# Performance work log

Measured on AMD Instinct MI355X. Metric: run time of the kernel, lower is better.

The kernel has to match this reference:

```python
import jax, jax.numpy as jnp
import numpy as np

B, T, I, H, L = 32768, 30, 4, 64, 32


def _lstm_layer(x, Wih, Whh, bih, bhh):
    """PyTorch-semantics single-layer LSTM, batch_first. Returns (outputs [B,T,H], h_T [B,H])."""
    # Precompute input contribution for all timesteps: [B, T, 4H]
    xg = jnp.einsum('bti,gi->btg', x, Wih) + bih + bhh
    Hh = Whh.shape[1]
    h0 = jnp.zeros((x.shape[0], Hh), x.dtype)

    def step(carry, xg_t):
        h, c = carry
        g = xg_t + h @ Whh.T  # [B, 4H]
        i, f, gg, o = jnp.split(g, 4, axis=-1)  # PyTorch gate order i,f,g,o
        c = jax.nn.sigmoid(f) * c + jax.nn.sigmoid(i) * jnp.tanh(gg)
        h = jax.nn.sigmoid(o) * jnp.tanh(c)
        return (h, c), h

    (hT, _), hs = jax.lax.scan(step, (h0, h0), jnp.swapaxes(xg, 0, 1))
    return jnp.swapaxes(hs, 0, 1), hT


def setup_inputs() -> dict:
    key = jax.random.key(0)
    ks = jax.random.split(key, 20)
    s = 0.1  # weight scale for numerical stability
    inp = {
        'x': jax.random.normal(ks[0], (B, T, I), jnp.float32),
        'enc1_Wih': s * jax.random.normal(ks[1], (4 * H, I), jnp.float32),
        'enc1_Whh': s * jax.random.normal(ks[2], (4 * H, H), jnp.float32),
        'enc1_bih': s * jax.random.normal(ks[3], (4 * H,), jnp.float32),
        'enc1_bhh': s * jax.random.normal(ks[4], (4 * H,), jnp.float32),
        'enc2_Wih': s * jax.random.normal(ks[5], (4 * L, H), jnp.float32),
        'enc2_Whh': s * jax.random.normal(ks[6], (4 * L, L), jnp.float32),
        'enc2_bih': s * jax.random.normal(ks[7], (4 * L,), jnp.float32),
        'enc2_bhh': s * jax.random.normal(ks[8], (4 * L,), jnp.float32),
        'dec1_Wih': s * jax.random.normal(ks[9], (4 * H, L), jnp.float32),
        'dec1_Whh': s * jax.random.normal(ks[10], (4 * H, H), jnp.float32),
        'dec1_bih': s * jax.random.normal(ks[11], (4 * H,), jnp.float32),
        'dec1_bhh': s * jax.random.normal(ks[12], (4 * H,), jnp.float32),
        'dec2_Wih': s * jax.random.normal(ks[13], (4 * I, H), jnp.float32),
        'dec2_Whh': s * jax.random.normal(ks[14], (4 * I, I), jnp.float32),
        'dec2_bih': s * jax.random.normal(ks[15], (4 * I,), jnp.float32),
        'dec2_bhh': s * jax.random.normal(ks[16], (4 * I,), jnp.float32),
    }
    return inp


def reference(x, enc1_Wih, enc1_Whh, enc1_bih, enc1_bhh,
              enc2_Wih, enc2_Whh, enc2_bih, enc2_bhh,
              dec1_Wih, dec1_Whh, dec1_bih, dec1_bhh,
              dec2_Wih, dec2_Whh, dec2_bih, dec2_bhh):
    seq_len = x.shape[1]
    out, _ = _lstm_layer(x, enc1_Wih, enc1_Whh, enc1_bih, enc1_bhh)
    out, h = _lstm_layer(out, enc2_Wih, enc2_Whh, enc2_bih, enc2_bhh)
    latent = jnp.repeat(h[:, None, :], seq_len, axis=1)  # [B, T, L]
    out, _ = _lstm_layer(latent, dec1_Wih, dec1_Whh, dec1_bih, dec1_bhh)
    out, _ = _lstm_layer(out, dec2_Wih, dec2_Whh, dec2_bih, dec2_bhh)
    return out
```

## Files before the change

### kernel.cpp

```cpp
#include <hip/hip_runtime.h>
#include <stdint.h>


typedef unsigned short u16;
typedef unsigned int u32;
typedef __attribute__((ext_vector_type(8))) short bf16x8;
typedef __attribute__((ext_vector_type(4))) short s16x4;
typedef __attribute__((ext_vector_type(4))) float f32x4;

#define BATCH 32768
#define TT 30
#define IN 4
#define WAVES 16
#define BLOCKT (WAVES * 64)
#define MB 16
#define NPAIR 8
#define BPB (NPAIR * MB)

#define LOG2E 1.4426950408889634f
#define LOG2E2 2.8853900817779268f

#define WREG 18432
#define O_WHH1HI 0
#define O_W1FOLD 8192
#define O_WIH2HI 12288
#define O_WHH2HI 16384
#define O_WHH3HI 0
#define O_WIH3HI 8192
#define O_WIH4HI 12288
#define O_W4HHF  12800

#define NBIAS 400
#define PBUF 1600
#define SMEM_WORDS (WREG + NBIAS + NPAIR * PBUF)
#define SMEM_BYTES (SMEM_WORDS * 4)

#define WB() __builtin_amdgcn_wave_barrier()
#define MFMA(a, b, c) __builtin_amdgcn_mfma_f32_16x16x32_bf16((a), (b), (c), 0, 0, 0)

__device__ __forceinline__ u16 f2bf(float f) {
    u32 u = __float_as_uint(f);
    u += 0x7fffu + ((u >> 16) & 1u);
    return (u16)(u >> 16);
}
__device__ __forceinline__ float bf2f(u16 v) { return __uint_as_float(((u32)v) << 16); }
__device__ __forceinline__ float sigY(float y) {
    return __builtin_amdgcn_rcpf(1.f + __builtin_amdgcn_exp2f(-y));
}
__device__ __forceinline__ float tanhY(float y) {
    return fmaf(-2.f, __builtin_amdgcn_rcpf(__builtin_amdgcn_exp2f(y) + 1.f), 1.f);
}
__device__ __forceinline__ float tanhC(float c) { return tanhY(c * LOG2E2); }

template <int KT, int GS>
__device__ __forceinline__ void stageBh(u16* hi, const float* src, int N, int tid) {
    const int K = KT * 32;
    const int total = N * K;
    for (int idx = tid; idx < total; idx += BLOCKT) {
        const int j = idx & 7;
        const int l = (idx >> 3) & 63;
        const int pr = idx >> 9;
        const int kt = pr & (KT - 1);
        const int nt = pr / KT;
        const int n = (nt << 4) | (l & 15);
        const int k = (kt << 5) + ((l >> 4) << 3) + j;
        const float s = (((n >> GS) & 3) == 2) ? LOG2E2 : LOG2E;
        hi[idx] = f2bf(src[n * K + k] * s);
    }
}

__device__ __forceinline__ f32x4 splat4(float b) {
    f32x4 v = {b, b, b, b};
    return v;
}

__global__ __launch_bounds__(BLOCKT)
__attribute__((amdgpu_waves_per_eu(4, 4)))
void lstm_ae(
    const float* __restrict__ x,
    const float* __restrict__ w1ih, const float* __restrict__ w1hh,
    const float* __restrict__ b1i, const float* __restrict__ b1h,
    const float* __restrict__ w2ih, const float* __restrict__ w2hh,
    const float* __restrict__ b2i, const float* __restrict__ b2h,
    const float* __restrict__ w3ih, const float* __restrict__ w3hh,
    const float* __restrict__ b3i, const float* __restrict__ b3h,
    const float* __restrict__ w4ih, const float* __restrict__ w4hh,
    const float* __restrict__ b4i, const float* __restrict__ b4h,
    float* __restrict__ out) {
    extern __shared__ float smem[];
    float* W = smem;
    float* biasF = smem + WREG;
    float* bufs = biasF + NBIAS;

    const int tid = threadIdx.x;
    const int wave = tid >> 6, lane = tid & 63;
    const int pair = wave & 7, role = wave >> 3;
    const int col = lane & 15, quad = lane >> 4;

    float* pb = bufs + pair * PBUF;
    u16* h1d = (u16*)pb;
    u16* h2b = (u16*)(pb + 1024);
    u16* xfold = (u16*)(pb + 1280);
    float* gbuf = pb + 1280;
    float* bufH4 = pb + 1536;

    const int b0w = blockIdx.x * BPB + pair * MB;

    stageBh<2, 6>((u16*)(W + O_WHH1HI), w1hh, 256, tid);
    stageBh<2, 5>((u16*)(W + O_WIH2HI), w2ih, 128, tid);
    stageBh<1, 5>((u16*)(W + O_WHH2HI), w2hh, 128, tid);
    {
        u16* F = (u16*)(W + O_W1FOLD);
        for (int idx = tid; idx < 16 * 512; idx += BLOCKT) {
            const int nt = idx >> 9;
            const int rem = idx & 511;
            const int l = rem >> 3;
            const int j = rem & 7;
            const int q = l >> 4;
            const int n = (nt << 4) | (l & 15);
            const float s = ((n >> 6) == 2) ? LOG2E2 : LOG2E;
            u16 v = 0;
            if (q == 0) {
                v = f2bf(w1ih[n * 4 + (j & 3)] * s);
            } else if (q == 1) {
                if (j < 4) {
                    const float w = w1ih[n * 4 + j] * s;
                    v = f2bf(w - bf2f(f2bf(w)));
                } else if (j == 4) {
                    v = f2bf((b1i[n] + b1h[n]) * s);
                } else if (j == 5) {
                    const float b = (b1i[n] + b1h[n]) * s;
                    v = f2bf(b - bf2f(f2bf(b)));
                }
            }
            F[idx] = v;
        }
    }
    for (int i = tid; i < 128; i += BLOCKT)
        biasF[i] = (b2i[i] + b2h[i]) * ((((i >> 5) & 3) == 2) ? LOG2E2 : LOG2E);
    for (int i = tid; i < 256; i += BLOCKT)
        biasF[128 + i] = (b3i[i] + b3h[i]) * ((((i >> 6) & 3) == 2) ? LOG2E2 : LOG2E);
    for (int i = tid; i < 16; i += BLOCKT)
        biasF[384 + i] = (b4i[i] + b4h[i]) * ((((i >> 2) & 3) == 2) ? LOG2E2 : LOG2E);
    {
        u32* z = (u32*)pb;
        if (role == 0) {
            for (int i = lane; i < 1024; i += 64) z[i] = 0u;
            for (int i = lane; i < 256; i += 64) z[1280 + i] = 0u;
        } else {
            for (int i = lane; i < 256; i += 64) z[1024 + i] = 0u;
            if (lane < 64) bufH4[lane] = 0.f;
        }
    }
    WB();
    if (role == 0 && quad == 1) {
        xfold[lane * 8 + 4] = (u16)0x3F80;
        xfold[lane * 8 + 5] = (u16)0x3F80;
    }
    __syncthreads();

    const u16* Whh1hi = (const u16*)(W + O_WHH1HI);
    const u16* W1fold = (const u16*)(W + O_W1FOLD);
    const u16* Wih2hi = (const u16*)(W + O_WIH2HI);
    const u16* Whh2hi = (const u16*)(W + O_WHH2HI);

    float c1[4][4];
    float c2[2][4];
#pragma unroll
    for (int q = 0; q < 4; ++q)
#pragma unroll
        for (int r = 0; r < 4; ++r) c1[q][r] = 0.f;
#pragma unroll
    for (int q = 0; q < 2; ++q)
#pragma unroll
        for (int r = 0; r < 4; ++r) c2[q][r] = 0.f;

    const f32x4 zf = {0.f, 0.f, 0.f, 0.f};
    float4 xcur;
    if (role == 0)
        xcur = *reinterpret_cast<const float4*>(x + ((size_t)(b0w + col) * TT + 0) * IN);

    for (int s = 0; s <= TT; ++s) {
        if (role == 0) {
            if (s < TT) {
                {
                    const u16 xh0 = f2bf(xcur.x), xh1 = f2bf(xcur.y);
                    const u16 xh2 = f2bf(xcur.z), xh3 = f2bf(xcur.w);
                    if (quad == 0) {
                        bf16x8 v;
                        v[0] = (short)xh0; v[1] = (short)xh1; v[2] = (short)xh2; v[3] = (short)xh3;
                        v[4] = (short)f2bf(xcur.x - bf2f(xh0));
                        v[5] = (short)f2bf(xcur.y - bf2f(xh1));
                        v[6] = (short)f2bf(xcur.z - bf2f(xh2));
                        v[7] = (short)f2bf(xcur.w - bf2f(xh3));
                        *reinterpret_cast<bf16x8*>(xfold + lane * 8) = v;
                    } else if (quad == 1) {
                        s16x4 v;
                        v[0] = (short)xh0; v[1] = (short)xh1; v[2] = (short)xh2; v[3] = (short)xh3;
                        *reinterpret_cast<s16x4*>(xfold + lane * 8) = v;
                    }
                }
                WB();
                {
                    const int tn = (s + 1 < TT) ? s + 1 : s;
                    xcur = *reinterpret_cast<const float4*>(
                        x + ((size_t)(b0w + col) * TT + tn) * IN);
                }
                const u16* hprev = h1d + (((s + 1) & 1) << 10);
                u16* hout = h1d + ((s & 1) << 10);
                const bf16x8 a1h0 = *reinterpret_cast<const bf16x8*>(hprev + lane * 8);
                const bf16x8 a1h1 = *reinterpret_cast<const bf16x8*>(hprev + (64 + lane) * 8);
                const bf16x8 a1x = *reinterpret_cast<const bf16x8*>(xfold + lane * 8);
#pragma unroll
                for (int q = 0; q < 4; ++q) {
                    f32x4 acc[4];
#pragma unroll
                    for (int i = 0; i < 4; ++i) {
                        const int nt = i * 4 + q;
                        const bf16x8 bx = *reinterpret_cast<const bf16x8*>(W1fold + (nt * 64 + lane) * 8);
                        const bf16x8 bh0 = *reinterpret_cast<const bf16x8*>(Whh1hi + ((nt * 2 + 0) * 64 + lane) * 8);
                        const bf16x8 bh1 = *reinterpret_cast<const bf16x8*>(Whh1hi + ((nt * 2 + 1) * 64 + lane) * 8);
                        f32x4 a = MFMA(a1x, bx, zf);
                        a = MFMA(a1h0, bh0, a);
                        a = MFMA(a1h1, bh1, a);
                        acc[i] = a;
                    }
                    const int kt = q >> 1;
                    const int lup = ((((q & 1) << 1) + (col >> 3)) << 4);
                    const int j = col & 7;
#pragma unroll
                    for (int r = 0; r < 4; ++r) {
                        const int m = quad * 4 + r;
                        const float iv = sigY(acc[0][r]);
                        const float fv = sigY(acc[1][r]);
                        const float gv = tanhY(acc[2][r]);
                        const float ov = sigY(acc[3][r]);
                        c1[q][r] = fv * c1[q][r] + iv * gv;
                        const float h = ov * tanhC(c1[q][r]);
                        hout[(kt * 64 + m + lup) * 8 + j] = f2bf(h);
                    }
                }
            }
        } else {
            if (s >= 1) {
                const u16* hprev = h1d + (((s + 1) & 1) << 10);
                const bf16x8 a1h0 = *reinterpret_cast<const bf16x8*>(hprev + lane * 8);
                const bf16x8 a1h1 = *reinterpret_cast<const bf16x8*>(hprev + (64 + lane) * 8);
                const bf16x8 a2h = *reinterpret_cast<const bf16x8*>(h2b + lane * 8);
                f32x4 acc2[8];
#pragma unroll
                for (int nt = 0; nt < 8; ++nt) {
                    const bf16x8 bh0 = *reinterpret_cast<const bf16x8*>(Wih2hi + ((nt * 2 + 0) * 64 + lane) * 8);
                    const bf16x8 bh1 = *reinterpret_cast<const bf16x8*>(Wih2hi + ((nt * 2 + 1) * 64 + lane) * 8);
                    const bf16x8 ch = *reinterpret_cast<const bf16x8*>(Whh2hi + (nt * 64 + lane) * 8);
                    f32x4 a = splat4(biasF[nt * 16 + col]);
                    a = MFMA(a1h0, bh0, a);
                    a = MFMA(a1h1, bh1, a);
                    a = MFMA(a2h, ch, a);
                    acc2[nt] = a;
                }
                WB();
#pragma unroll
                for (int q = 0; q < 2; ++q) {
                    const int lup = (((q << 1) + (col >> 3)) << 4);
                    const int j = col & 7;
#pragma unroll
                    for (int r = 0; r < 4; ++r) {
                        const int m = quad * 4 + r;
                        const float iv = sigY(acc2[q][r]);
                        const float fv = sigY(acc2[2 + q][r]);
                        const float gv = tanhY(acc2[4 + q][r]);
                        const float ov = sigY(acc2[6 + q][r]);
                        c2[q][r] = fv * c2[q][r] + iv * gv;
                        const float h = ov * tanhC(c2[q][r]);
                        h2b[(m + lup) * 8 + j] = f2bf(h);
                    }
                }
            }
        }
        __syncthreads();
    }

    stageBh<2, 6>((u16*)(W + O_WHH3HI), w3hh, 256, tid);
    stageBh<1, 6>((u16*)(W + O_WIH3HI), w3ih, 256, tid);
    stageBh<2, 2>((u16*)(W + O_WIH4HI), w4ih, 16, tid);
    for (int i = tid; i < 64; i += BLOCKT)
        W[O_W4HHF + i] = w4hh[i] * ((((i >> 4) & 3) == 2) ? LOG2E2 : LOG2E);
    if (role == 0) {
        u32* z = (u32*)pb;
        for (int i = lane; i < 1024; i += 64) z[i] = 0u;
    } else {
        if (lane < 64) bufH4[lane] = 0.f;
    }
    __syncthreads();

    const u16* Whh3hi = (const u16*)(W + O_WHH3HI);
    const u16* Wih3hi = (const u16*)(W + O_WIH3HI);
    const u16* Wih4hi = (const u16*)(W + O_WIH4HI);
    const float* W4hhF = W + O_W4HHF;

    float c3[4][4];
    float c4 = 0.f, bias4r = 0.f;
    bf16x8 aLh;
    if (role == 0) {
#pragma unroll
        for (int q = 0; q < 4; ++q)
#pragma unroll
            for (int r = 0; r < 4; ++r) c3[q][r] = 0.f;
        aLh = *reinterpret_cast<const bf16x8*>(h2b + lane * 8);
    } else {
        bias4r = biasF[384 + col];
    }
    const int u4 = lane & 3, mb = lane >> 2;

    for (int s = 0; s <= TT; ++s) {
        if (role == 0) {
            if (s < TT) {
                const u16* hprev = h1d + (((s + 1) & 1) << 10);
                u16* hout = h1d + ((s & 1) << 10);
                const bf16x8 a3h0 = *reinterpret_cast<const bf16x8*>(hprev + lane * 8);
                const bf16x8 a3h1 = *reinterpret_cast<const bf16x8*>(hprev + (64 + lane) * 8);
#pragma unroll
                for (int q = 0; q < 4; ++q) {
                    f32x4 acc[4];
#pragma unroll
                    for (int i = 0; i < 4; ++i) {
                        const int nt = i * 4 + q;
                        const bf16x8 bL = *reinterpret_cast<const bf16x8*>(Wih3hi + (nt * 64 + lane) * 8);
                        const bf16x8 bh0 = *reinterpret_cast<const bf16x8*>(Whh3hi + ((nt * 2 + 0) * 64 + lane) * 8);
                        const bf16x8 bh1 = *reinterpret_cast<const bf16x8*>(Whh3hi + ((nt * 2 + 1) * 64 + lane) * 8);
                        f32x4 a = MFMA(aLh, bL, splat4(biasF[128 + nt * 16 + col]));
                        a = MFMA(a3h0, bh0, a);
                        a = MFMA(a3h1, bh1, a);
                        acc[i] = a;
                    }
                    const int kt = q >> 1;
                    const int lup = ((((q & 1) << 1) + (col >> 3)) << 4);
                    const int j = col & 7;
#pragma unroll
                    for (int r = 0; r < 4; ++r) {
                        const int m = quad * 4 + r;
                        const float iv = sigY(acc[0][r]);
                        const float fv = sigY(acc[1][r]);
                        const float gv = tanhY(acc[2][r]);
                        const float ov = sigY(acc[3][r]);
                        c3[q][r] = fv * c3[q][r] + iv * gv;
                        const float h = ov * tanhC(c3[q][r]);
                        hout[(kt * 64 + m + lup) * 8 + j] = f2bf(h);
                    }
                }
            }
        } else {
            if (s >= 1) {
                const int t = s - 1;
                const u16* hprev = h1d + (((s + 1) & 1) << 10);
                const bf16x8 a3h0 = *reinterpret_cast<const bf16x8*>(hprev + lane * 8);
                const bf16x8 a3h1 = *reinterpret_cast<const bf16x8*>(hprev + (64 + lane) * 8);
                f32x4 acc4 = splat4(bias4r);
                {
                    const float4 w4 = *reinterpret_cast<const float4*>(W4hhF + col * 4);
#pragma unroll
                    for (int r = 0; r < 4; ++r) {
                        const float4 hv = *reinterpret_cast<const float4*>(bufH4 + (quad * 4 + r) * 4);
                        float sa = acc4[r];
                        sa = fmaf(w4.x, hv.x, sa);
                        sa = fmaf(w4.y, hv.y, sa);
                        sa = fmaf(w4.z, hv.z, sa);
                        sa = fmaf(w4.w, hv.w, sa);
                        acc4[r] = sa;
                    }
                }
                {
                    const bf16x8 bh0 = *reinterpret_cast<const bf16x8*>(Wih4hi + (0 * 64 + lane) * 8);
                    const bf16x8 bh1 = *reinterpret_cast<const bf16x8*>(Wih4hi + (1 * 64 + lane) * 8);
                    acc4 = MFMA(a3h0, bh0, acc4);
                    acc4 = MFMA(a3h1, bh1, acc4);
                }
                WB();
#pragma unroll
                for (int r = 0; r < 4; ++r) gbuf[(quad * 4 + r) * 16 + col] = acc4[r];
                WB();
                {
                    const float iv = sigY(gbuf[mb * 16 + u4]);
                    const float fv = sigY(gbuf[mb * 16 + 4 + u4]);
                    const float gv = tanhY(gbuf[mb * 16 + 8 + u4]);
                    const float ov = sigY(gbuf[mb * 16 + 12 + u4]);
                    c4 = fv * c4 + iv * gv;
                    const float h = ov * tanhC(c4);
                    out[((size_t)(b0w + mb) * TT + t) * IN + u4] = h;
                    bufH4[mb * 4 + u4] = h;
                }
                WB();
            }
        }
        __syncthreads();
    }
}

extern "C" void kernel_launch(void* const* d_in, const int* in_sizes, int n_in,
                              void* d_out, int out_size, void* d_ws, size_t ws_size,
                              hipStream_t stream) {
    (void)in_sizes; (void)n_in; (void)d_ws; (void)ws_size; (void)out_size;
    hipFuncSetAttribute(reinterpret_cast<const void*>(lstm_ae),
                        hipFuncAttributeMaxDynamicSharedMemorySize, SMEM_BYTES);
    const float* xi = (const float*)d_in[0];
    const float* w1ih = (const float*)d_in[1];
    const float* w1hh = (const float*)d_in[2];
    const float* b1i = (const float*)d_in[3];
    const float* b1h = (const float*)d_in[4];
    const float* w2ih = (const float*)d_in[5];
    const float* w2hh = (const float*)d_in[6];
    const float* b2i = (const float*)d_in[7];
    const float* b2h = (const float*)d_in[8];
    const float* w3ih = (const float*)d_in[9];
    const float* w3hh = (const float*)d_in[10];
    const float* b3i = (const float*)d_in[11];
    const float* b3h = (const float*)d_in[12];
    const float* w4ih = (const float*)d_in[13];
    const float* w4hh = (const float*)d_in[14];
    const float* b4i = (const float*)d_in[15];
    const float* b4h = (const float*)d_in[16];
    float* out = (float*)d_out;

    lstm_ae<<<dim3(BATCH / BPB), dim3(BLOCKT), SMEM_BYTES, stream>>>(
        xi, w1ih, w1hh, b1i, b1h, w2ih, w2hh, b2i, b2h,
        w3ih, w3hh, b3i, b3h, w4ih, w4hh, b4i, b4h, out);
}
```

Measured before the change: 311.2 us.

## Split LSTM layer work across both waves of a pair instead of layer pipelining

Before, each wave pair ran a two-stage pipeline: one wave computed layer 1 (or 3) while the other computed layer 2 (or 4) one step behind. Now both waves share each layer's hidden units, half the gate columns each, and the layers run one after the other inside each timestep with an extra __syncthreads between them. Layer 2's hidden state becomes double-buffered, so the per-pair shared buffer grows. This balances the per-wave MFMA load, since layer 1 was much heavier than layer 2. The cost is two block barriers per step and a serial dependency between the layers within a step, and layer 4 still runs on only one wave.

```diff
diff --git a/kernel.cpp b/kernel.cpp
--- a/kernel.cpp
+++ b/kernel.cpp
@@ -31,7 +31,7 @@
 #define O_W4HHF  12800
 
 #define NBIAS 400
-#define PBUF 1600
+#define PBUF 1856
 #define SMEM_WORDS (WREG + NBIAS + NPAIR * PBUF)
 #define SMEM_BYTES (SMEM_WORDS * 4)
 
@@ -98,11 +98,11 @@
     const int col = lane & 15, quad = lane >> 4;
 
     float* pb = bufs + pair * PBUF;
-    u16* h1d = (u16*)pb;
-    u16* h2b = (u16*)(pb + 1024);
-    u16* xfold = (u16*)(pb + 1280);
-    float* gbuf = pb + 1280;
-    float* bufH4 = pb + 1536;
+    u16* h1u = (u16*)pb;
+    u16* h2u = (u16*)(pb + 1024);
+    u16* xfold = (u16*)(pb + 1536);
+    float* gbuf = pb + 1536;
+    float* bufH4 = pb + 1792;
 
     const int b0w = blockIdx.x * BPB + pair * MB;
 
@@ -146,10 +146,9 @@
         u32* z = (u32*)pb;
         if (role == 0) {
             for (int i = lane; i < 1024; i += 64) z[i] = 0u;
-            for (int i = lane; i < 256; i += 64) z[1280 + i] = 0u;
+            for (int i = lane; i < 256; i += 64) z[1536 + i] = 0u;
         } else {
-            for (int i = lane; i < 256; i += 64) z[1024 + i] = 0u;
-            if (lane < 64) bufH4[lane] = 0.f;
+            for (int i = lane; i < 512; i += 64) z[1024 + i] = 0u;
         }
     }
     WB();
@@ -164,118 +163,113 @@
     const u16* Wih2hi = (const u16*)(W + O_WIH2HI);
     const u16* Whh2hi = (const u16*)(W + O_WHH2HI);
 
-    float c1[4][4];
-    float c2[2][4];
-#pragma unroll
-    for (int q = 0; q < 4; ++q)
-#pragma unroll
-        for (int r = 0; r < 4; ++r) c1[q][r] = 0.f;
-#pragma unroll
-    for (int q = 0; q < 2; ++q)
-#pragma unroll
-        for (int r = 0; r < 4; ++r) c2[q][r] = 0.f;
+    float c1[2][4];
+    float c2[4];
+#pragma unroll
+    for (int qi = 0; qi < 2; ++qi)
+#pragma unroll
+        for (int r = 0; r < 4; ++r) c1[qi][r] = 0.f;
+#pragma unroll
+    for (int r = 0; r < 4; ++r) c2[r] = 0.f;
 
     const f32x4 zf = {0.f, 0.f, 0.f, 0.f};
-    float4 xcur;
-    if (role == 0)
-        xcur = *reinterpret_cast<const float4*>(x + ((size_t)(b0w + col) * TT + 0) * IN);
-
-    for (int s = 0; s <= TT; ++s) {
-        if (role == 0) {
-            if (s < TT) {
-                {
-                    const u16 xh0 = f2bf(xcur.x), xh1 = f2bf(xcur.y);
-                    const u16 xh2 = f2bf(xcur.z), xh3 = f2bf(xcur.w);
-                    if (quad == 0) {
-                        bf16x8 v;
-                        v[0] = (short)xh0; v[1] = (short)xh1; v[2] = (short)xh2; v[3] = (short)xh3;
-                        v[4] = (short)f2bf(xcur.x - bf2f(xh0));
-                        v[5] = (short)f2bf(xcur.y - bf2f(xh1));
-                        v[6] = (short)f2bf(xcur.z - bf2f(xh2));
-                        v[7] = (short)f2bf(xcur.w - bf2f(xh3));
-                        *reinterpret_cast<bf16x8*>(xfold + lane * 8) = v;
-                    } else if (quad == 1) {
-                        s16x4 v;
-                        v[0] = (short)xh0; v[1] = (short)xh1; v[2] = (short)xh2; v[3] = (short)xh3;
-                        *reinterpret_cast<s16x4*>(xfold + lane * 8) = v;
-                    }
-                }
-                WB();
-                {
-                    const int tn = (s + 1 < TT) ? s + 1 : s;
-                    xcur = *reinterpret_cast<const float4*>(
-                        x + ((size_t)(b0w + col) * TT + tn) * IN);
-                }
-                const u16* hprev = h1d + (((s + 1) & 1) << 10);
-                u16* hout = h1d + ((s & 1) << 10);
-                const bf16x8 a1h0 = *reinterpret_cast<const bf16x8*>(hprev + lane * 8);
-                const bf16x8 a1h1 = *reinterpret_cast<const bf16x8*>(hprev + (64 + lane) * 8);
-                const bf16x8 a1x = *reinterpret_cast<const bf16x8*>(xfold + lane * 8);
-#pragma unroll
-                for (int q = 0; q < 4; ++q) {
-                    f32x4 acc[4];
-#pragma unroll
-                    for (int i = 0; i < 4; ++i) {
-                        const int nt = i * 4 + q;
-                        const bf16x8 bx = *reinterpret_cast<const bf16x8*>(W1fold + (nt * 64 + lane) * 8);
-                        const bf16x8 bh0 = *reinterpret_cast<const bf16x8*>(Whh1hi + ((nt * 2 + 0) * 64 + lane) * 8);
-                        const bf16x8 bh1 = *reinterpret_cast<const bf16x8*>(Whh1hi + ((nt * 2 + 1) * 64 + lane) * 8);
-                        f32x4 a = MFMA(a1x, bx, zf);
-                        a = MFMA(a1h0, bh0, a);
-                        a = MFMA(a1h1, bh1, a);
-                        acc[i] = a;
-                    }
-                    const int kt = q >> 1;
-                    const int lup = ((((q & 1) << 1) + (col >> 3)) << 4);
-                    const int j = col & 7;
-#pragma unroll
-                    for (int r = 0; r < 4; ++r) {
-                        const int m = quad * 4 + r;
-                        const float iv = sigY(acc[0][r]);
-                        const float fv = sigY(acc[1][r]);
-                        const float gv = tanhY(acc[2][r]);
-                        const float ov = sigY(acc[3][r]);
-                        c1[q][r] = fv * c1[q][r] + iv * gv;
-                        const float h = ov * tanhC(c1[q][r]);
-                        hout[(kt * 64 + m + lup) * 8 + j] = f2bf(h);
-                    }
-                }
-            }
-        } else {
-            if (s >= 1) {
-                const u16* hprev = h1d + (((s + 1) & 1) << 10);
-                const bf16x8 a1h0 = *reinterpret_cast<const bf16x8*>(hprev + lane * 8);
-                const bf16x8 a1h1 = *reinterpret_cast<const bf16x8*>(hprev + (64 + lane) * 8);
-                const bf16x8 a2h = *reinterpret_cast<const bf16x8*>(h2b + lane * 8);
-                f32x4 acc2[8];
-#pragma unroll
-                for (int nt = 0; nt < 8; ++nt) {
-                    const bf16x8 bh0 = *reinterpret_cast<const bf16x8*>(Wih2hi + ((nt * 2 + 0) * 64 + lane) * 8);
-                    const bf16x8 bh1 = *reinterpret_cast<const bf16x8*>(Wih2hi + ((nt * 2 + 1) * 64 + lane) * 8);
-                    const bf16x8 ch = *reinterpret_cast<const bf16x8*>(Whh2hi + (nt * 64 + lane) * 8);
-                    f32x4 a = splat4(biasF[nt * 16 + col]);
+    float4 xcur = *reinterpret_cast<const float4*>(
+        x + ((size_t)(b0w + col) * TT + 0) * IN);
+
+    for (int t = 0; t < TT; ++t) {
+        {
+            const u16 xh0 = f2bf(xcur.x), xh1 = f2bf(xcur.y);
+            const u16 xh2 = f2bf(xcur.z), xh3 = f2bf(xcur.w);
+            if (quad == 0) {
+                bf16x8 v;
+                v[0] = (short)xh0; v[1] = (short)xh1; v[2] = (short)xh2; v[3] = (short)xh3;
+                v[4] = (short)f2bf(xcur.x - bf2f(xh0));
+                v[5] = (short)f2bf(xcur.y - bf2f(xh1));
+                v[6] = (short)f2bf(xcur.z - bf2f(xh2));
+                v[7] = (short)f2bf(xcur.w - bf2f(xh3));
+                *reinterpret_cast<bf16x8*>(xfold + lane * 8) = v;
+            } else if (quad == 1) {
+                s16x4 v;
+                v[0] = (short)xh0; v[1] = (short)xh1; v[2] = (short)xh2; v[3] = (short)xh3;
+                *reinterpret_cast<s16x4*>(xfold + lane * 8) = v;
+            }
+        }
+        WB();
+        {
+            const int tn = (t + 1 < TT) ? t + 1 : t;
+            xcur = *reinterpret_cast<const float4*>(
+                x + ((size_t)(b0w + col) * TT + tn) * IN);
+        }
+        {
+            const u16* hp = h1u + (((t + 1) & 1) << 10);
+            u16* ho = h1u + ((t & 1) << 10);
+            const bf16x8 a1h0 = *reinterpret_cast<const bf16x8*>(hp + lane * 8);
+            const bf16x8 a1h1 = *reinterpret_cast<const bf16x8*>(hp + (64 + lane) * 8);
+            const bf16x8 a1x = *reinterpret_cast<const bf16x8*>(xfold + lane * 8);
+#pragma unroll
+            for (int qi = 0; qi < 2; ++qi) {
+                const int q = role * 2 + qi;
+                f32x4 acc[4];
+#pragma unroll
+                for (int g = 0; g < 4; ++g) {
+                    const int nt = g * 4 + q;
+                    const bf16x8 bx = *reinterpret_cast<const bf16x8*>(W1fold + (nt * 64 + lane) * 8);
+                    const bf16x8 bh0 = *reinterpret_cast<const bf16x8*>(Whh1hi + ((nt * 2 + 0) * 64 + lane) * 8);
+                    const bf16x8 bh1 = *reinterpret_cast<const bf16x8*>(Whh1hi + ((nt * 2 + 1) * 64 + lane) * 8);
+                    f32x4 a = MFMA(a1x, bx, zf);
                     a = MFMA(a1h0, bh0, a);
                     a = MFMA(a1h1, bh1, a);
-                    a = MFMA(a2h, ch, a);
-                    acc2[nt] = a;
-                }
-                WB();
-#pragma unroll
-                for (int q = 0; q < 2; ++q) {
-                    const int lup = (((q << 1) + (col >> 3)) << 4);
-                    const int j = col & 7;
-#pragma unroll
-                    for (int r = 0; r < 4; ++r) {
-                        const int m = quad * 4 + r;
-                        const float iv = sigY(acc2[q][r]);
-                        const float fv = sigY(acc2[2 + q][r]);
-                        const float gv = tanhY(acc2[4 + q][r]);
-                        const float ov = sigY(acc2[6 + q][r]);
-                        c2[q][r] = fv * c2[q][r] + iv * gv;
-                        const float h = ov * tanhC(c2[q][r]);
-                        h2b[(m + lup) * 8 + j] = f2bf(h);
-                    }
-                }
+                    acc[g] = a;
+                }
+                const int kt = q >> 1;
+                const int lup = ((((q & 1) << 1) + (col >> 3)) << 4);
+                const int j = col & 7;
+#pragma unroll
+                for (int r = 0; r < 4; ++r) {
+                    const int m = quad * 4 + r;
+                    const float iv = sigY(acc[0][r]);
+                    const float fv = sigY(acc[1][r]);
+                    const float gv = tanhY(acc[2][r]);
+                    const float ov = sigY(acc[3][r]);
+                    c1[qi][r] = fv * c1[qi][r] + iv * gv;
+                    const float h = ov * tanhC(c1[qi][r]);
+                    ho[(kt * 64 + m + lup) * 8 + j] = f2bf(h);
+                }
+            }
+        }
+        __syncthreads();
+        {
+            const u16* h1n = h1u + ((t & 1) << 10);
+            const u16* h2p = h2u + (((t + 1) & 1) << 9);
+            u16* h2o = h2u + ((t & 1) << 9);
+            const bf16x8 a1h0 = *reinterpret_cast<const bf16x8*>(h1n + lane * 8);
+            const bf16x8 a1h1 = *reinterpret_cast<const bf16x8*>(h1n + (64 + lane) * 8);
+            const bf16x8 a2h = *reinterpret_cast<const bf16x8*>(h2p + lane * 8);
+            f32x4 acc[4];
+#pragma unroll
+            for (int g = 0; g < 4; ++g) {
+                const int nt2 = g * 2 + role;
+                const bf16x8 bh0 = *reinterpret_cast<const bf16x8*>(Wih2hi + ((nt2 * 2 + 0) * 64 + lane) * 8);
+                const bf16x8 bh1 = *reinterpret_cast<const bf16x8*>(Wih2hi + ((nt2 * 2 + 1) * 64 + lane) * 8);
+                const bf16x8 ch = *reinterpret_cast<const bf16x8*>(Whh2hi + (nt2 * 64 + lane) * 8);
+                f32x4 a = splat4(biasF[nt2 * 16 + col]);
+                a = MFMA(a1h0, bh0, a);
+                a = MFMA(a1h1, bh1, a);
+                a = MFMA(a2h, ch, a);
+                acc[g] = a;
+            }
+            const int lup2 = ((role * 2 + (col >> 3)) << 4);
+            const int j = col & 7;
+#pragma unroll
+            for (int r = 0; r < 4; ++r) {
+                const int m = quad * 4 + r;
+                const float iv = sigY(acc[0][r]);
+                const float fv = sigY(acc[1][r]);
+                const float gv = tanhY(acc[2][r]);
+                const float ov = sigY(acc[3][r]);
+                c2[r] = fv * c2[r] + iv * gv;
+                const float h = ov * tanhC(c2[r]);
+                h2o[(m + lup2) * 8 + j] = f2bf(h);
             }
         }
         __syncthreads();
@@ -299,99 +293,94 @@
     const u16* Wih4hi = (const u16*)(W + O_WIH4HI);
     const float* W4hhF = W + O_W4HHF;
 
-    float c3[4][4];
-    float c4 = 0.f, bias4r = 0.f;
-    bf16x8 aLh;
-    if (role == 0) {
-#pragma unroll
-        for (int q = 0; q < 4; ++q)
-#pragma unroll
-            for (int r = 0; r < 4; ++r) c3[q][r] = 0.f;
-        aLh = *reinterpret_cast<const bf16x8*>(h2b + lane * 8);
-    } else {
-        bias4r = biasF[384 + col];
-    }
+    const bf16x8 aLh = *reinterpret_cast<const bf16x8*>(
+        h2u + (((TT - 1) & 1) << 9) + lane * 8);
+    float c3[2][4];
+#pragma unroll
+    for (int qi = 0; qi < 2; ++qi)
+#pragma unroll
+        for (int r = 0; r < 4; ++r) c3[qi][r] = 0.f;
+    float c4 = 0.f;
+    const float bias4r = biasF[384 + col];
     const int u4 = lane & 3, mb = lane >> 2;
 
-    for (int s = 0; s <= TT; ++s) {
-        if (role == 0) {
-            if (s < TT) {
-                const u16* hprev = h1d + (((s + 1) & 1) << 10);
-                u16* hout = h1d + ((s & 1) << 10);
-                const bf16x8 a3h0 = *reinterpret_cast<const bf16x8*>(hprev + lane * 8);
-                const bf16x8 a3h1 = *reinterpret_cast<const bf16x8*>(hprev + (64 + lane) * 8);
-#pragma unroll
-                for (int q = 0; q < 4; ++q) {
-                    f32x4 acc[4];
-#pragma unroll
-                    for (int i = 0; i < 4; ++i) {
-                        const int nt = i * 4 + q;
-                        const bf16x8 bL = *reinterpret_cast<const bf16x8*>(Wih3hi + (nt * 64 + lane) * 8);
-                        const bf16x8 bh0 = *reinterpret_cast<const bf16x8*>(Whh3hi + ((nt * 2 + 0) * 64 + lane) * 8);
-                        const bf16x8 bh1 = *reinterpret_cast<const bf16x8*>(Whh3hi + ((nt * 2 + 1) * 64 + lane) * 8);
-                        f32x4 a = MFMA(aLh, bL, splat4(biasF[128 + nt * 16 + col]));
-                        a = MFMA(a3h0, bh0, a);
-                        a = MFMA(a3h1, bh1, a);
-                        acc[i] = a;
-                    }
-                    const int kt = q >> 1;
-                    const int lup = ((((q & 1) << 1) + (col >> 3)) << 4);
-                    const int j = col & 7;
-#pragma unroll
-                    for (int r = 0; r < 4; ++r) {
-                        const int m = quad * 4 + r;
-                        const float iv = sigY(acc[0][r]);
-                        const float fv = sigY(acc[1][r]);
-                        const float gv = tanhY(acc[2][r]);
-                        const float ov = sigY(acc[3][r]);
-                        c3[q][r] = fv * c3[q][r] + iv * gv;
-                        const float h = ov * tanhC(c3[q][r]);
-                        hout[(kt * 64 + m + lup) * 8 + j] = f2bf(h);
-                    }
-                }
-            }
-        } else {
-            if (s >= 1) {
-                const int t = s - 1;
-                const u16* hprev = h1d + (((s + 1) & 1) << 10);
-                const bf16x8 a3h0 = *reinterpret_cast<const bf16x8*>(hprev + lane * 8);
-                const bf16x8 a3h1 = *reinterpret_cast<const bf16x8*>(hprev + (64 + lane) * 8);
-                f32x4 acc4 = splat4(bias4r);
-                {
-                    const float4 w4 = *reinterpret_cast<const float4*>(W4hhF + col * 4);
-#pragma unroll
-                    for (int r = 0; r < 4; ++r) {
-                        const float4 hv = *reinterpret_cast<const float4*>(bufH4 + (quad * 4 + r) * 4);
-                        float sa = acc4[r];
-                        sa = fmaf(w4.x, hv.x, sa);
-                        sa = fmaf(w4.y, hv.y, sa);
-                        sa = fmaf(w4.z, hv.z, sa);
-                        sa = fmaf(w4.w, hv.w, sa);
-                        acc4[r] = sa;
-                    }
-                }
-                {
-                    const bf16x8 bh0 = *reinterpret_cast<const bf16x8*>(Wih4hi + (0 * 64 + lane) * 8);
-                    const bf16x8 bh1 = *reinterpret_cast<const bf16x8*>(Wih4hi + (1 * 64 + lane) * 8);
-                    acc4 = MFMA(a3h0, bh0, acc4);
-                    acc4 = MFMA(a3h1, bh1, acc4);
-                }
-                WB();
-#pragma unroll
-                for (int r = 0; r < 4; ++r) gbuf[(quad * 4 + r) * 16 + col] = acc4[r];
-                WB();
-                {
-                    const float iv = sigY(gbuf[mb * 16 + u4]);
-                    const float fv = sigY(gbuf[mb * 16 + 4 + u4]);
-                    const float gv = tanhY(gbuf[mb * 16 + 8 + u4]);
-                    const float ov = sigY(gbuf[mb * 16 + 12 + u4]);
-                    c4 = fv * c4 + iv * gv;
-                    const float h = ov * tanhC(c4);
-                    out[((size_t)(b0w + mb) * TT + t) * IN + u4] = h;
-                    bufH4[mb * 4 + u4] = h;
-                }
-                WB();
-            }
+    for (int t = 0; t < TT; ++t) {
+        {
+            const u16* hp = h1u + (((t + 1) & 1) << 10);
+            u16* ho = h1u + ((t & 1) << 10);
+            const bf16x8 a3h0 = *reinterpret_cast<const bf16x8*>(hp + lane * 8);
+            const bf16x8 a3h1 = *reinterpret_cast<const bf16x8*>(hp + (64 + lane) * 8);
+#pragma unroll
+            for (int qi = 0; qi < 2; ++qi) {
+                const int q = role * 2 + qi;
+                f32x4 acc[4];
+#pragma unroll
+                for (int g = 0; g < 4; ++g) {
+                    const int nt = g * 4 + q;
+                    const bf16x8 bL = *reinterpret_cast<const bf16x8*>(Wih3hi + (nt * 64 + lane) * 8);
+                    const bf16x8 bh0 = *reinterpret_cast<const bf16x8*>(Whh3hi + ((nt * 2 + 0) * 64 + lane) * 8);
+                    const bf16x8 bh1 = *reinterpret_cast<const bf16x8*>(Whh3hi + ((nt * 2 + 1) * 64 + lane) * 8);
+                    f32x4 a = MFMA(aLh, bL, splat4(biasF[128 + nt * 16 + col]));
+                    a = MFMA(a3h0, bh0, a);
+                    a = MFMA(a3h1, bh1, a);
+                    acc[g] = a;
+                }
+                const int kt = q >> 1;
+                const int lup = ((((q & 1) << 1) + (col >> 3)) << 4);
+                const int j = col & 7;
+#pragma unroll
+                for (int r = 0; r < 4; ++r) {
+                    const int m = quad * 4 + r;
+                    const float iv = sigY(acc[0][r]);
+                    const float fv = sigY(acc[1][r]);
+                    const float gv = tanhY(acc[2][r]);
+                    const float ov = sigY(acc[3][r]);
+                    c3[qi][r] = fv * c3[qi][r] + iv * gv;
+                    const float h = ov * tanhC(c3[qi][r]);
+                    ho[(kt * 64 + m + lup) * 8 + j] = f2bf(h);
+                }
+            }
+        }
+        __syncthreads();
+        if (role == 1) {
+            const u16* h3n = h1u + ((t & 1) << 10);
+            const bf16x8 a3h0 = *reinterpret_cast<const bf16x8*>(h3n + lane * 8);
+            const bf16x8 a3h1 = *reinterpret_cast<const bf16x8*>(h3n + (64 + lane) * 8);
+            f32x4 acc4 = splat4(bias4r);
+            {
+                const float4 w4 = *reinterpret_cast<const float4*>(W4hhF + col * 4);
+#pragma unroll
+                for (int r = 0; r < 4; ++r) {
+                    const float4 hv = *reinterpret_cast<const float4*>(bufH4 + (quad * 4 + r) * 4);
+                    float sa = acc4[r];
+                    sa = fmaf(w4.x, hv.x, sa);
+                    sa = fmaf(w4.y, hv.y, sa);
+                    sa = fmaf(w4.z, hv.z, sa);
+                    sa = fmaf(w4.w, hv.w, sa);
+                    acc4[r] = sa;
+                }
+            }
+            {
+                const bf16x8 bh0 = *reinterpret_cast<const bf16x8*>(Wih4hi + (0 * 64 + lane) * 8);
+                const bf16x8 bh1 = *reinterpret_cast<const bf16x8*>(Wih4hi + (1 * 64 + lane) * 8);
+                acc4 = MFMA(a3h0, bh0, acc4);
+                acc4 = MFMA(a3h1, bh1, acc4);
+            }
+            WB();
+#pragma unroll
+            for (int r = 0; r < 4; ++r) gbuf[(quad * 4 + r) * 16 + col] = acc4[r];
+            WB();
+            {
+                const float iv = sigY(gbuf[mb * 16 + u4]);
+                const float fv = sigY(gbuf[mb * 16 + 4 + u4]);
+                const float gv = tanhY(gbuf[mb * 16 + 8 + u4]);
+                const float ov = sigY(gbuf[mb * 16 + 12 + u4]);
+                c4 = fv * c4 + iv * gv;
+                const float h = ov * tanhC(c4);
+                out[((size_t)(b0w + mb) * TT + t) * IN + u4] = h;
+                bufH4[mb * 4 + u4] = h;
+            }
+            WB();
         }
         __syncthreads();
     }
```

After: 331.9 us. +6.7%, slower.
